# Optimization experiments

Hardware: AMD Instinct MI355X
Metric: run time of the kernel (lower is better)

## Reference

```python
import jax, jax.numpy as jnp
import numpy as np

DIM = 512
NUM_HEADS = 8
HEAD_DIM = DIM // NUM_HEADS
SCALE = HEAD_DIM ** -0.5


def setup_inputs() -> dict:
    key = jax.random.key(0)
    k_x, k_qkv, k_proj, k_pb = jax.random.split(key, 4)
    x = jax.random.normal(k_x, (2, 4096, DIM), dtype=jnp.float32)
    # nn.Linear weights: stored as [out, in]; qkv_bias=False so no qkv bias.
    w_qkv = jax.random.normal(k_qkv, (3 * DIM, DIM), dtype=jnp.float32) * (DIM ** -0.5)
    w_proj = jax.random.normal(k_proj, (DIM, DIM), dtype=jnp.float32) * (DIM ** -0.5)
    b_proj = jax.random.normal(k_pb, (DIM,), dtype=jnp.float32) * 0.01
    return {"x": x, "w_qkv": w_qkv, "w_proj": w_proj, "b_proj": b_proj}


def reference(x, w_qkv, w_proj, b_proj):
    B, N, D = x.shape
    H, Hd = NUM_HEADS, HEAD_DIM
    # qkv: [B, N, 3D] -> [3, B, H, N, Hd]
    qkv = (x @ w_qkv.T).reshape(B, N, 3, H, Hd).transpose(2, 0, 3, 1, 4)
    q, k, v = qkv[0], qkv[1], qkv[2]
    # Naive full attention matrix in fp32 (matches original non-fused path).
    attn = jnp.einsum('bhqd,bhkd->bhqk', q, k) * SCALE
    attn = jax.nn.softmax(attn, axis=-1)
    out = jnp.einsum('bhqk,bhkd->bhqd', attn, v)
    out = out.transpose(0, 2, 1, 3).reshape(B, N, D)
    return out @ w_proj.T + b_proj
```

## Files before the change

### kernel.cpp

```cpp
#include <hip/hip_runtime.h>
#include <stdint.h>

#define SEQ   4096
#define DIMM  512
#define HDIM  64
#define NH    8
#define ROWS  8192
#define QKVN  1536

typedef __attribute__((ext_vector_type(8))) __bf16 bf16x8;
typedef __attribute__((ext_vector_type(4))) float  f32x4;
typedef __attribute__((ext_vector_type(4))) uint32_t u32x4;

__device__ __forceinline__ uint32_t cvtpk(float lo, float hi) {
  uint32_t w;
  asm("v_cvt_pk_bf16_f32 %0, %1, %2" : "=v"(w) : "v"(lo), "v"(hi));
  return w;
}

__device__ __forceinline__ void swap32(uint32_t& a, uint32_t& b) {
  asm("v_permlane32_swap_b32 %0, %1" : "+v"(a), "+v"(b));
}
__device__ __forceinline__ void swap16(uint32_t& a, uint32_t& b) {
  asm("v_permlane16_swap_b32 %0, %1" : "+v"(a), "+v"(b));
}

__device__ __forceinline__ f32x4 mfma16(bf16x8 a, bf16x8 b, f32x4 c) {
  return __builtin_amdgcn_mfma_f32_16x16x32_bf16(a, b, c, 0, 0, 0);
}

#if __has_builtin(__builtin_amdgcn_exp2f)
#define EXP2F(x) __builtin_amdgcn_exp2f(x)
#else
#define EXP2F(x) exp2f(x)
#endif

__device__ __forceinline__ void gld16(const void* g, void* l) {
  __builtin_amdgcn_global_load_lds(
      (const __attribute__((address_space(1))) uint32_t*)g,
      (__attribute__((address_space(3))) uint32_t*)l, 16, 0, 0);
}

#define X4  (ROWS * DIMM / 4)
#define Q4  (QKVN * DIMM / 4)
#define P4  (DIMM * DIMM / 4)

__global__ __launch_bounds__(256) void cvt_kernel(
    const float* __restrict__ x, const float* __restrict__ wq,
    const float* __restrict__ wp, uint16_t* __restrict__ xb,
    uint16_t* __restrict__ wqb, uint16_t* __restrict__ wpb) {
  int idx = blockIdx.x * 256 + threadIdx.x;
  const float* src; uint16_t* dst; int i4;
  if (idx < X4)            { src = x;  dst = xb;  i4 = idx; }
  else if (idx < X4 + Q4)  { src = wq; dst = wqb; i4 = idx - X4; }
  else                     { src = wp; dst = wpb; i4 = idx - X4 - Q4; }
  float4 v = ((const float4*)src)[i4];
  uint2 o;
  o.x = cvtpk(v.x, v.y);
  o.y = cvtpk(v.z, v.w);
  ((uint2*)dst)[i4] = o;
}

__device__ __forceinline__ void gemm_core(
    const uint16_t* __restrict__ A, const uint16_t* __restrict__ B,
    uint16_t (*As)[128 * 32], uint16_t (*Bs)[128 * 32], f32x4 acc[4][4]) {
  const int tid = threadIdx.x;
  const int lane = tid & 63, wave = tid >> 6;
  const int quad = lane >> 4, l16 = lane & 15;
  const int wr = (wave & 1) * 64, wc = (wave >> 1) * 64;
  const int bm = blockIdx.x, bn = blockIdx.y;
  const int sw = (l16 >> 1) & 3;

  auto stage = [&](int buf, int kt) {
#pragma unroll
    for (int it = 0; it < 2; ++it) {
      int L = it * 256 + tid;
      int r = L >> 2, c = L & 3;
      int gc = c ^ ((r >> 1) & 3);
      int ldsoff = (it * 256 + (tid & ~63)) * 16;
      gld16((const char*)A + ((size_t)(bm * 128 + r) * DIMM + kt * 32) * 2 + gc * 16,
            (char*)As[buf] + ldsoff);
      gld16((const char*)B + ((size_t)(bn * 128 + r) * DIMM + kt * 32) * 2 + gc * 16,
            (char*)Bs[buf] + ldsoff);
    }
  };

  stage(0, 0);
  for (int kt = 0; kt < DIMM / 32; ++kt) {
    const int cur = kt & 1;
    __syncthreads();
    if (kt < DIMM / 32 - 1) stage(cur ^ 1, kt + 1);

    bf16x8 af[4], bfr[4];
#pragma unroll
    for (int i = 0; i < 4; ++i)
      af[i] = *(const bf16x8*)(As[cur] + (wr + i * 16 + l16) * 32 + ((quad ^ sw) * 8));
#pragma unroll
    for (int j = 0; j < 4; ++j)
      bfr[j] = *(const bf16x8*)(Bs[cur] + (wc + j * 16 + l16) * 32 + ((quad ^ sw) * 8));
    __builtin_amdgcn_s_setprio(1);
#pragma unroll
    for (int i = 0; i < 4; ++i)
#pragma unroll
      for (int j = 0; j < 4; ++j)
        acc[i][j] = mfma16(af[i], bfr[j], acc[i][j]);
    __builtin_amdgcn_s_setprio(0);
  }
}

__global__ __launch_bounds__(256, 4) void qkv_gemm(
    const uint16_t* __restrict__ xb, const uint16_t* __restrict__ wqb,
    uint16_t* __restrict__ qd, uint16_t* __restrict__ kd,
    uint16_t* __restrict__ vt) {
  __shared__ __align__(16) uint16_t As[2][128 * 32];
  __shared__ __align__(16) uint16_t Bs[2][128 * 32];
  f32x4 acc[4][4];
#pragma unroll
  for (int i = 0; i < 4; ++i)
#pragma unroll
    for (int j = 0; j < 4; ++j) acc[i][j] = f32x4{0.f, 0.f, 0.f, 0.f};

  gemm_core(xb, wqb, As, Bs, acc);

  const int lane = threadIdx.x & 63, wave = threadIdx.x >> 6;
  const int quad = lane >> 4, l16 = lane & 15;
  const int wr = (wave & 1) * 64, wc = (wave >> 1) * 64;
  const float qscale = 0.125f * 1.44269504f;
#pragma unroll
  for (int i = 0; i < 4; ++i) {
    int m0 = blockIdx.x * 128 + wr + i * 16 + quad * 4;
    int b = m0 >> 12, n0 = m0 & 4095;
#pragma unroll
    for (int j = 0; j < 4; ++j) {
      int jc = blockIdx.y * 128 + wc + j * 16 + l16;
      int region = jc >> 9;
      int h = (jc >> 6) & 7, hd = jc & 63;
      int bh = (b << 3) | h;
      if (region == 0) {
        uint32_t w01 = cvtpk(acc[i][j][0] * qscale, acc[i][j][1] * qscale);
        uint32_t w23 = cvtpk(acc[i][j][2] * qscale, acc[i][j][3] * qscale);
        size_t rb = ((size_t)bh * SEQ + n0) * HDIM + hd;
        qd[rb]            = (uint16_t)w01;
        qd[rb + HDIM]     = (uint16_t)(w01 >> 16);
        qd[rb + 2 * HDIM] = (uint16_t)w23;
        qd[rb + 3 * HDIM] = (uint16_t)(w23 >> 16);
      } else if (region == 1) {
        uint32_t w01 = cvtpk(acc[i][j][0], acc[i][j][1]);
        uint32_t w23 = cvtpk(acc[i][j][2], acc[i][j][3]);
        size_t rb = ((size_t)bh * SEQ + n0) * HDIM + hd;
        kd[rb]            = (uint16_t)w01;
        kd[rb + HDIM]     = (uint16_t)(w01 >> 16);
        kd[rb + 2 * HDIM] = (uint16_t)w23;
        kd[rb + 3 * HDIM] = (uint16_t)(w23 >> 16);
      } else {
        uint2 pk;
        pk.x = cvtpk(acc[i][j][0], acc[i][j][1]);
        pk.y = cvtpk(acc[i][j][2], acc[i][j][3]);
        *(uint2*)(vt + ((size_t)bh * HDIM + hd) * SEQ + n0) = pk;
      }
    }
  }
}

__global__ __launch_bounds__(512, 4) void attn_kernel(
    const uint16_t* __restrict__ qd, const uint16_t* __restrict__ kd,
    const uint16_t* __restrict__ vt, uint16_t* __restrict__ ao) {
  __shared__ __align__(16) uint16_t Ks[2][128 * 64];
  __shared__ __align__(16) uint16_t Vs[2][64 * 128];

  const int tid = threadIdx.x, lane = tid & 63, wave = tid >> 6;
  const int quad = lane >> 4, l16 = lane & 15;
  const int pair = wave >> 1, khalf = wave & 1;
  const int wid = blockIdx.x;
  const int xcd = wid & 7, slot = wid >> 3;
  const int bh = xcd + 8 * (slot & 1);
  const int qt = slot >> 1;
  const size_t base_qk = (size_t)bh * SEQ * HDIM;
  const size_t base_v  = (size_t)bh * HDIM * SEQ;
  const int sw7 = l16 & 7;

  auto stage = [&](int buf, int kt) {
#pragma unroll
    for (int it = 0; it < 2; ++it) {
      int L = it * 512 + tid;
      int ldsoff = (it * 512 + (tid & ~63)) * 16;
      int rk = L >> 3, ck = L & 7;
      int gck = ck ^ (rk & 7);
      gld16((const char*)kd + (base_qk + (size_t)(kt * 128 + rk) * HDIM) * 2 + gck * 16,
            (char*)Ks[buf] + ldsoff);
      int rv = L >> 4, cv = L & 15;
      int gcv = cv ^ (rv & 15);
      gld16((const char*)vt + (base_v + (size_t)rv * SEQ + (size_t)kt * 128) * 2 + gcv * 16,
            (char*)Vs[buf] + ldsoff);
    }
  };

  bf16x8 qf[2][2];
#pragma unroll
  for (int it2 = 0; it2 < 2; ++it2)
#pragma unroll
    for (int kh = 0; kh < 2; ++kh)
      qf[it2][kh] = *(const bf16x8*)(qd + base_qk +
          (size_t)(qt * 128 + pair * 32 + it2 * 16 + l16) * HDIM + kh * 32 + quad * 8);

  f32x4 O[2][4];
  float lsum[2] = {0.f, 0.f};
#pragma unroll
  for (int a = 0; a < 2; ++a)
#pragma unroll
    for (int d = 0; d < 4; ++d) O[a][d] = f32x4{0.f, 0.f, 0.f, 0.f};

  stage(0, 0);
  for (int kt = 0; kt < SEQ / 128; ++kt) {
    const int cur = kt & 1;
    __syncthreads();
    if (kt < SEQ / 128 - 1) stage(cur ^ 1, kt + 1);

    bf16x8 kf[4][2];
#pragma unroll
    for (int jh = 0; jh < 4; ++jh) {
      int jf = khalf * 4 + jh;
      const uint16_t* krow = Ks[cur] + (jf * 16 + l16) * 64;
      kf[jh][0] = *(const bf16x8*)(krow + ((quad ^ sw7) * 8));
      kf[jh][1] = *(const bf16x8*)(krow + (((4 + quad) ^ sw7) * 8));
    }

    f32x4 P[4][2];
    __builtin_amdgcn_s_setprio(1);
#pragma unroll
    for (int jh = 0; jh < 4; ++jh)
#pragma unroll
      for (int it2 = 0; it2 < 2; ++it2) {
        f32x4 s = f32x4{0.f, 0.f, 0.f, 0.f};
        s = mfma16(kf[jh][0], qf[it2][0], s);
        s = mfma16(kf[jh][1], qf[it2][1], s);
        P[jh][it2] = s;
      }
    __builtin_amdgcn_s_setprio(0);

    uint32_t sp[4][2][2];
#pragma unroll
    for (int jh = 0; jh < 4; ++jh)
#pragma unroll
      for (int it2 = 0; it2 < 2; ++it2) {
        float p0 = EXP2F(P[jh][it2][0]);
        float p1 = EXP2F(P[jh][it2][1]);
        float p2 = EXP2F(P[jh][it2][2]);
        float p3 = EXP2F(P[jh][it2][3]);
        lsum[it2] += (p0 + p1) + (p2 + p3);
        sp[jh][it2][0] = cvtpk(p0, p1);
        sp[jh][it2][1] = cvtpk(p2, p3);
      }

    bf16x8 pb[2][2];
#pragma unroll
    for (int kp = 0; kp < 2; ++kp)
#pragma unroll
      for (int it2 = 0; it2 < 2; ++it2) {
        uint32_t t0 = sp[2 * kp][it2][0], t2 = sp[2 * kp + 1][it2][0];
        swap32(t0, t2); swap16(t0, t2);
        uint32_t t1 = sp[2 * kp][it2][1], t3 = sp[2 * kp + 1][it2][1];
        swap32(t1, t3); swap16(t1, t3);
        u32x4 w = {t0, t1, t2, t3};
        pb[kp][it2] = __builtin_bit_cast(bf16x8, w);
      }

#pragma unroll
    for (int kp = 0; kp < 2; ++kp) {
      bf16x8 va[4];
#pragma unroll
      for (int dl = 0; dl < 4; ++dl)
        va[dl] = *(const bf16x8*)((const char*)Vs[cur] + (dl * 16 + l16) * 256 +
                                  (((khalf * 8 + kp * 4 + quad) ^ l16) & 15) * 16);
      __builtin_amdgcn_s_setprio(1);
#pragma unroll
      for (int it2 = 0; it2 < 2; ++it2)
#pragma unroll
        for (int dl = 0; dl < 4; ++dl)
          O[it2][dl] = mfma16(va[dl], pb[kp][it2], O[it2][dl]);
      __builtin_amdgcn_s_setprio(0);
    }
  }

  __syncthreads();
  if (!(wave & 1)) {
    f32x4* ob = (f32x4*)((char*)Ks + pair * 8192);
#pragma unroll
    for (int it2 = 0; it2 < 2; ++it2)
#pragma unroll
      for (int dl = 0; dl < 4; ++dl)
        ob[(it2 * 4 + dl) * 64 + lane] = O[it2][dl];
    float2* lb = (float2*)((char*)Vs + pair * 512);
    lb[lane] = make_float2(lsum[0], lsum[1]);
  }
  __syncthreads();
  if (wave & 1) {
    const f32x4* ob = (const f32x4*)((char*)Ks + pair * 8192);
    float2 lp = ((const float2*)((char*)Vs + pair * 512))[lane];
    lsum[0] += lp.x; lsum[1] += lp.y;
#pragma unroll
    for (int it2 = 0; it2 < 2; ++it2)
#pragma unroll
      for (int dl = 0; dl < 4; ++dl)
        O[it2][dl] += ob[(it2 * 4 + dl) * 64 + lane];

    const int b = bh >> 3, h = bh & 7;
#pragma unroll
    for (int it2 = 0; it2 < 2; ++it2) {
      float l = lsum[it2];
      l += __shfl_xor(l, 16);
      l += __shfl_xor(l, 32);
      float inv = 1.0f / l;
      int q = qt * 128 + pair * 32 + it2 * 16 + l16;
      size_t rowbase = ((size_t)(b * SEQ + q)) * DIMM + h * HDIM;
#pragma unroll
      for (int dl = 0; dl < 4; ++dl) {
        uint2 pk;
        pk.x = cvtpk(O[it2][dl][0] * inv, O[it2][dl][1] * inv);
        pk.y = cvtpk(O[it2][dl][2] * inv, O[it2][dl][3] * inv);
        *(uint2*)(ao + rowbase + dl * 16 + quad * 4) = pk;
      }
    }
  }
}

__global__ __launch_bounds__(256, 4) void proj_gemm(
    const uint16_t* __restrict__ ao, const uint16_t* __restrict__ wpb,
    const float* __restrict__ bprj, float* __restrict__ out) {
  __shared__ __align__(16) uint16_t As[2][128 * 32];
  __shared__ __align__(16) uint16_t Bs[2][128 * 32];
  f32x4 acc[4][4];
#pragma unroll
  for (int i = 0; i < 4; ++i)
#pragma unroll
    for (int j = 0; j < 4; ++j) acc[i][j] = f32x4{0.f, 0.f, 0.f, 0.f};

  gemm_core(ao, wpb, As, Bs, acc);

  const int lane = threadIdx.x & 63, wave = threadIdx.x >> 6;
  const int quad = lane >> 4, l16 = lane & 15;
  const int wr = (wave & 1) * 64, wc = (wave >> 1) * 64;
#pragma unroll
  for (int i = 0; i < 4; ++i) {
    int m0 = blockIdx.x * 128 + wr + i * 16 + quad * 4;
#pragma unroll
    for (int j = 0; j < 4; ++j) {
      int jc = blockIdx.y * 128 + wc + j * 16 + l16;
      float bias = bprj[jc];
#pragma unroll
      for (int r = 0; r < 4; ++r)
        out[(size_t)(m0 + r) * DIMM + jc] = acc[i][j][r] + bias;
    }
  }
}

extern "C" void kernel_launch(void* const* d_in, const int* in_sizes, int n_in,
                              void* d_out, int out_size, void* d_ws, size_t ws_size,
                              hipStream_t stream) {
  const float* x     = (const float*)d_in[0];
  const float* wqkv  = (const float*)d_in[1];
  const float* wproj = (const float*)d_in[2];
  const float* bproj = (const float*)d_in[3];

  char* ws = (char*)d_ws;
  uint16_t* xb  = (uint16_t*)(ws + 0);
  uint16_t* wqb = (uint16_t*)(ws + 8388608);
  uint16_t* wpb = (uint16_t*)(ws + 9961472);
  uint16_t* qd  = (uint16_t*)(ws + 10485760);
  uint16_t* kd  = (uint16_t*)(ws + 18874368);
  uint16_t* vt  = (uint16_t*)(ws + 27262976);
  uint16_t* ao  = (uint16_t*)(ws + 35651584);

  cvt_kernel<<<(X4 + Q4 + P4) / 256, 256, 0, stream>>>(x, wqkv, wproj, xb, wqb, wpb);
  qkv_gemm<<<dim3(64, 12), 256, 0, stream>>>(xb, wqb, qd, kd, vt);
  attn_kernel<<<512, 512, 0, stream>>>(qd, kd, vt, ao);
  proj_gemm<<<dim3(64, 4), 256, 0, stream>>>(ao, wpb, bproj, (float*)d_out);
}
```

Before: 183.4 us.

## Software-pipeline attention K/V loads with split staging, and remap GEMM tiles per XCD

The attention loop now stages K and V separately and keeps K two tiles ahead. The QK^T for tile t+1 is computed while the exp/pack for tile t runs, using explicit vmcnt waits and raw barriers in place of __syncthreads. This is meant to overlap global loads with MFMA and exp work and to cut barrier stalls. The QKV and projection GEMMs also remap the linear block index so tiles sharing the same row panel land on the same XCD, for better L2 reuse. The hand-counted waitcnts add a correctness risk if the in-flight load counts are wrong.

New measurement: 573.1 us. +212.5%, slower.

```diff
diff --git a/kernel.cpp b/kernel.cpp
--- a/kernel.cpp
+++ b/kernel.cpp
@@ -7,6 +7,7 @@
 #define NH    8
 #define ROWS  8192
 #define QKVN  1536
+#define NT    (SEQ / 128)
 
 typedef __attribute__((ext_vector_type(8))) __bf16 bf16x8;
 typedef __attribute__((ext_vector_type(4))) float  f32x4;
@@ -40,6 +41,12 @@
       (const __attribute__((address_space(1))) uint32_t*)g,
       (__attribute__((address_space(3))) uint32_t*)l, 16, 0, 0);
 }
+
+#define WAIT_BAR(N) do {                                      \
+    asm volatile("s_waitcnt vmcnt(" #N ")" ::: "memory");     \
+    __builtin_amdgcn_s_barrier();                             \
+    __builtin_amdgcn_sched_barrier(0);                        \
+  } while (0)
 
 #define X4  (ROWS * DIMM / 4)
 #define Q4  (QKVN * DIMM / 4)
@@ -62,13 +69,13 @@
 }
 
 __device__ __forceinline__ void gemm_core(
+    int bm, int bn,
     const uint16_t* __restrict__ A, const uint16_t* __restrict__ B,
     uint16_t (*As)[128 * 32], uint16_t (*Bs)[128 * 32], f32x4 acc[4][4]) {
   const int tid = threadIdx.x;
   const int lane = tid & 63, wave = tid >> 6;
   const int quad = lane >> 4, l16 = lane & 15;
   const int wr = (wave & 1) * 64, wc = (wave >> 1) * 64;
-  const int bm = blockIdx.x, bn = blockIdx.y;
   const int sw = (l16 >> 1) & 3;
 
   auto stage = [&](int buf, int kt) {
@@ -114,13 +121,16 @@
     uint16_t* __restrict__ vt) {
   __shared__ __align__(16) uint16_t As[2][128 * 32];
   __shared__ __align__(16) uint16_t Bs[2][128 * 32];
+  const int lin = blockIdx.y * 64 + blockIdx.x;
+  const int bm = (lin & 7) * 8 + ((lin >> 3) / 12);
+  const int bn = (lin >> 3) % 12;
   f32x4 acc[4][4];
 #pragma unroll
   for (int i = 0; i < 4; ++i)
 #pragma unroll
     for (int j = 0; j < 4; ++j) acc[i][j] = f32x4{0.f, 0.f, 0.f, 0.f};
 
-  gemm_core(xb, wqb, As, Bs, acc);
+  gemm_core(bm, bn, xb, wqb, As, Bs, acc);
 
   const int lane = threadIdx.x & 63, wave = threadIdx.x >> 6;
   const int quad = lane >> 4, l16 = lane & 15;
@@ -128,11 +138,11 @@
   const float qscale = 0.125f * 1.44269504f;
 #pragma unroll
   for (int i = 0; i < 4; ++i) {
-    int m0 = blockIdx.x * 128 + wr + i * 16 + quad * 4;
+    int m0 = bm * 128 + wr + i * 16 + quad * 4;
     int b = m0 >> 12, n0 = m0 & 4095;
 #pragma unroll
     for (int j = 0; j < 4; ++j) {
-      int jc = blockIdx.y * 128 + wc + j * 16 + l16;
+      int jc = bn * 128 + wc + j * 16 + l16;
       int region = jc >> 9;
       int h = (jc >> 6) & 7, hd = jc & 63;
       int bh = (b << 3) | h;
@@ -179,19 +189,26 @@
   const size_t base_v  = (size_t)bh * HDIM * SEQ;
   const int sw7 = l16 & 7;
 
-  auto stage = [&](int buf, int kt) {
+  auto stageK = [&](int sl, int kt) {
 #pragma unroll
     for (int it = 0; it < 2; ++it) {
       int L = it * 512 + tid;
-      int ldsoff = (it * 512 + (tid & ~63)) * 16;
       int rk = L >> 3, ck = L & 7;
       int gck = ck ^ (rk & 7);
+      int ldsoff = (it * 512 + (tid & ~63)) * 16;
       gld16((const char*)kd + (base_qk + (size_t)(kt * 128 + rk) * HDIM) * 2 + gck * 16,
-            (char*)Ks[buf] + ldsoff);
+            (char*)Ks[sl] + ldsoff);
+    }
+  };
+  auto stageV = [&](int sl, int kt) {
+#pragma unroll
+    for (int it = 0; it < 2; ++it) {
+      int L = it * 512 + tid;
       int rv = L >> 4, cv = L & 15;
       int gcv = cv ^ (rv & 15);
+      int ldsoff = (it * 512 + (tid & ~63)) * 16;
       gld16((const char*)vt + (base_v + (size_t)rv * SEQ + (size_t)kt * 128) * 2 + gcv * 16,
-            (char*)Vs[buf] + ldsoff);
+            (char*)Vs[sl] + ldsoff);
     }
   };
 
@@ -210,48 +227,39 @@
 #pragma unroll
     for (int d = 0; d < 4; ++d) O[a][d] = f32x4{0.f, 0.f, 0.f, 0.f};
 
-  stage(0, 0);
-  for (int kt = 0; kt < SEQ / 128; ++kt) {
-    const int cur = kt & 1;
-    __syncthreads();
-    if (kt < SEQ / 128 - 1) stage(cur ^ 1, kt + 1);
-
-    bf16x8 kf[4][2];
+  auto qkt = [&](int sl, f32x4 (&P)[4][2]) {
 #pragma unroll
     for (int jh = 0; jh < 4; ++jh) {
       int jf = khalf * 4 + jh;
-      const uint16_t* krow = Ks[cur] + (jf * 16 + l16) * 64;
-      kf[jh][0] = *(const bf16x8*)(krow + ((quad ^ sw7) * 8));
-      kf[jh][1] = *(const bf16x8*)(krow + (((4 + quad) ^ sw7) * 8));
-    }
-
-    f32x4 P[4][2];
-    __builtin_amdgcn_s_setprio(1);
-#pragma unroll
-    for (int jh = 0; jh < 4; ++jh)
+      const uint16_t* krow = Ks[sl] + (jf * 16 + l16) * 64;
+      bf16x8 kf0 = *(const bf16x8*)(krow + ((quad ^ sw7) * 8));
+      bf16x8 kf1 = *(const bf16x8*)(krow + (((4 + quad) ^ sw7) * 8));
 #pragma unroll
       for (int it2 = 0; it2 < 2; ++it2) {
         f32x4 s = f32x4{0.f, 0.f, 0.f, 0.f};
-        s = mfma16(kf[jh][0], qf[it2][0], s);
-        s = mfma16(kf[jh][1], qf[it2][1], s);
+        s = mfma16(kf0, qf[it2][0], s);
+        s = mfma16(kf1, qf[it2][1], s);
         P[jh][it2] = s;
       }
-    __builtin_amdgcn_s_setprio(0);
-
-    uint32_t sp[4][2][2];
+    }
+  };
+
+  auto expPack = [&](f32x4 (&Pc)[4][2], uint32_t (&sp)[4][2][2]) {
 #pragma unroll
     for (int jh = 0; jh < 4; ++jh)
 #pragma unroll
       for (int it2 = 0; it2 < 2; ++it2) {
-        float p0 = EXP2F(P[jh][it2][0]);
-        float p1 = EXP2F(P[jh][it2][1]);
-        float p2 = EXP2F(P[jh][it2][2]);
-        float p3 = EXP2F(P[jh][it2][3]);
+        float p0 = EXP2F(Pc[jh][it2][0]);
+        float p1 = EXP2F(Pc[jh][it2][1]);
+        float p2 = EXP2F(Pc[jh][it2][2]);
+        float p3 = EXP2F(Pc[jh][it2][3]);
         lsum[it2] += (p0 + p1) + (p2 + p3);
         sp[jh][it2][0] = cvtpk(p0, p1);
         sp[jh][it2][1] = cvtpk(p2, p3);
       }
-
+  };
+
+  auto pvStep = [&](int sl, uint32_t (&sp)[4][2][2]) {
     bf16x8 pb[2][2];
 #pragma unroll
     for (int kp = 0; kp < 2; ++kp)
@@ -264,13 +272,12 @@
         u32x4 w = {t0, t1, t2, t3};
         pb[kp][it2] = __builtin_bit_cast(bf16x8, w);
       }
-
 #pragma unroll
     for (int kp = 0; kp < 2; ++kp) {
       bf16x8 va[4];
 #pragma unroll
       for (int dl = 0; dl < 4; ++dl)
-        va[dl] = *(const bf16x8*)((const char*)Vs[cur] + (dl * 16 + l16) * 256 +
+        va[dl] = *(const bf16x8*)((const char*)Vs[sl] + (dl * 16 + l16) * 256 +
                                   (((khalf * 8 + kp * 4 + quad) ^ l16) & 15) * 16);
       __builtin_amdgcn_s_setprio(1);
 #pragma unroll
@@ -280,6 +287,29 @@
           O[it2][dl] = mfma16(va[dl], pb[kp][it2], O[it2][dl]);
       __builtin_amdgcn_s_setprio(0);
     }
+  };
+
+  auto stagestep = [&](int t, f32x4 (&Pc)[4][2], f32x4 (&Pn)[4][2]) {
+    WAIT_BAR(2);
+    if (t + 2 < NT) stageK(t & 1, t + 2);
+    uint32_t sp[4][2][2];
+    if (t + 1 < NT) qkt((t + 1) & 1, Pn);
+    expPack(Pc, sp);
+    if (t + 2 < NT) { WAIT_BAR(2); } else { WAIT_BAR(0); }
+    if (t + 1 < NT) stageV((t + 1) & 1, t + 1);
+    pvStep(t & 1, sp);
+  };
+
+  stageK(0, 0); stageK(1, 1); stageV(0, 0);
+  asm volatile("s_waitcnt vmcnt(4)" ::: "memory");
+  __builtin_amdgcn_s_barrier();
+  __builtin_amdgcn_sched_barrier(0);
+  f32x4 Pa[4][2], Pb[4][2];
+  qkt(0, Pa);
+
+  for (int t = 0; t < NT; t += 2) {
+    stagestep(t, Pa, Pb);
+    stagestep(t + 1, Pb, Pa);
   }
 
   __syncthreads();
@@ -329,23 +359,26 @@
     const float* __restrict__ bprj, float* __restrict__ out) {
   __shared__ __align__(16) uint16_t As[2][128 * 32];
   __shared__ __align__(16) uint16_t Bs[2][128 * 32];
+  const int lin = blockIdx.y * 64 + blockIdx.x;
+  const int bm = (lin & 7) * 8 + ((lin >> 3) >> 2);
+  const int bn = (lin >> 3) & 3;
   f32x4 acc[4][4];
 #pragma unroll
   for (int i = 0; i < 4; ++i)
 #pragma unroll
     for (int j = 0; j < 4; ++j) acc[i][j] = f32x4{0.f, 0.f, 0.f, 0.f};
 
-  gemm_core(ao, wpb, As, Bs, acc);
+  gemm_core(bm, bn, ao, wpb, As, Bs, acc);
 
   const int lane = threadIdx.x & 63, wave = threadIdx.x >> 6;
   const int quad = lane >> 4, l16 = lane & 15;
   const int wr = (wave & 1) * 64, wc = (wave >> 1) * 64;
 #pragma unroll
   for (int i = 0; i < 4; ++i) {
-    int m0 = blockIdx.x * 128 + wr + i * 16 + quad * 4;
+    int m0 = bm * 128 + wr + i * 16 + quad * 4;
 #pragma unroll
     for (int j = 0; j < 4; ++j) {
-      int jc = blockIdx.y * 128 + wc + j * 16 + l16;
+      int jc = bn * 128 + wc + j * 16 + l16;
       float bias = bprj[jc];
 #pragma unroll
       for (int r = 0; r < 4; ++r)
```

## Remap GEMM blocks for XCD locality and halve proj tile rows

Applied to the files above, without the earlier changes.

Both GEMMs now remap the linear block id so that consecutive blocks, which are spread round-robin across the 8 XCDs, share row tiles within an XCD, aiming to improve L2 reuse of A/B tiles. The projection GEMM switches to 64x128 tiles with each wave covering 32 columns, doubling the grid to 512 blocks so the 256-CU device is better filled. The smaller tile lowers per-block arithmetic intensity and adds more loads of the weight tile.

Measured after the change: 180.3 us. No clear change (-1.7%).

```diff
diff --git a/kernel.cpp b/kernel.cpp
--- a/kernel.cpp
+++ b/kernel.cpp
@@ -62,13 +62,13 @@
 }
 
 __device__ __forceinline__ void gemm_core(
+    int bm, int bn,
     const uint16_t* __restrict__ A, const uint16_t* __restrict__ B,
     uint16_t (*As)[128 * 32], uint16_t (*Bs)[128 * 32], f32x4 acc[4][4]) {
   const int tid = threadIdx.x;
   const int lane = tid & 63, wave = tid >> 6;
   const int quad = lane >> 4, l16 = lane & 15;
   const int wr = (wave & 1) * 64, wc = (wave >> 1) * 64;
-  const int bm = blockIdx.x, bn = blockIdx.y;
   const int sw = (l16 >> 1) & 3;
 
   auto stage = [&](int buf, int kt) {
@@ -114,13 +114,16 @@
     uint16_t* __restrict__ vt) {
   __shared__ __align__(16) uint16_t As[2][128 * 32];
   __shared__ __align__(16) uint16_t Bs[2][128 * 32];
+  const int lin = blockIdx.y * 64 + blockIdx.x;
+  const int bm = (lin & 7) * 8 + ((lin >> 3) / 12);
+  const int bn = (lin >> 3) % 12;
   f32x4 acc[4][4];
 #pragma unroll
   for (int i = 0; i < 4; ++i)
 #pragma unroll
     for (int j = 0; j < 4; ++j) acc[i][j] = f32x4{0.f, 0.f, 0.f, 0.f};
 
-  gemm_core(xb, wqb, As, Bs, acc);
+  gemm_core(bm, bn, xb, wqb, As, Bs, acc);
 
   const int lane = threadIdx.x & 63, wave = threadIdx.x >> 6;
   const int quad = lane >> 4, l16 = lane & 15;
@@ -128,11 +131,11 @@
   const float qscale = 0.125f * 1.44269504f;
 #pragma unroll
   for (int i = 0; i < 4; ++i) {
-    int m0 = blockIdx.x * 128 + wr + i * 16 + quad * 4;
+    int m0 = bm * 128 + wr + i * 16 + quad * 4;
     int b = m0 >> 12, n0 = m0 & 4095;
 #pragma unroll
     for (int j = 0; j < 4; ++j) {
-      int jc = blockIdx.y * 128 + wc + j * 16 + l16;
+      int jc = bn * 128 + wc + j * 16 + l16;
       int region = jc >> 9;
       int h = (jc >> 6) & 7, hd = jc & 63;
       int bh = (b << 3) | h;
@@ -327,25 +330,72 @@
 __global__ __launch_bounds__(256, 4) void proj_gemm(
     const uint16_t* __restrict__ ao, const uint16_t* __restrict__ wpb,
     const float* __restrict__ bprj, float* __restrict__ out) {
-  __shared__ __align__(16) uint16_t As[2][128 * 32];
+  __shared__ __align__(16) uint16_t As[2][64 * 32];
   __shared__ __align__(16) uint16_t Bs[2][128 * 32];
-  f32x4 acc[4][4];
+  const int lin = blockIdx.y * 128 + blockIdx.x;
+  const int idx = lin >> 3;
+  const int bm = (lin & 7) * 16 + (idx >> 2);
+  const int bn = idx & 3;
+
+  const int tid = threadIdx.x;
+  const int lane = tid & 63, wave = tid >> 6;
+  const int quad = lane >> 4, l16 = lane & 15;
+  const int wc = wave * 32;
+  const int sw = (l16 >> 1) & 3;
+
+  f32x4 acc[4][2];
 #pragma unroll
   for (int i = 0; i < 4; ++i)
 #pragma unroll
-    for (int j = 0; j < 4; ++j) acc[i][j] = f32x4{0.f, 0.f, 0.f, 0.f};
-
-  gemm_core(ao, wpb, As, Bs, acc);
-
-  const int lane = threadIdx.x & 63, wave = threadIdx.x >> 6;
-  const int quad = lane >> 4, l16 = lane & 15;
-  const int wr = (wave & 1) * 64, wc = (wave >> 1) * 64;
+    for (int j = 0; j < 2; ++j) acc[i][j] = f32x4{0.f, 0.f, 0.f, 0.f};
+
+  auto stage = [&](int buf, int kt) {
+    {
+      int r = tid >> 2, c = tid & 3;
+      int gc = c ^ ((r >> 1) & 3);
+      int ldsoff = (tid & ~63) * 16;
+      gld16((const char*)ao + ((size_t)(bm * 64 + r) * DIMM + kt * 32) * 2 + gc * 16,
+            (char*)As[buf] + ldsoff);
+    }
+#pragma unroll
+    for (int it = 0; it < 2; ++it) {
+      int L = it * 256 + tid;
+      int r = L >> 2, c = L & 3;
+      int gc = c ^ ((r >> 1) & 3);
+      int ldsoff = (it * 256 + (tid & ~63)) * 16;
+      gld16((const char*)wpb + ((size_t)(bn * 128 + r) * DIMM + kt * 32) * 2 + gc * 16,
+            (char*)Bs[buf] + ldsoff);
+    }
+  };
+
+  stage(0, 0);
+  for (int kt = 0; kt < DIMM / 32; ++kt) {
+    const int cur = kt & 1;
+    __syncthreads();
+    if (kt < DIMM / 32 - 1) stage(cur ^ 1, kt + 1);
+
+    bf16x8 af[4], bfr[2];
+#pragma unroll
+    for (int i = 0; i < 4; ++i)
+      af[i] = *(const bf16x8*)(As[cur] + (i * 16 + l16) * 32 + ((quad ^ sw) * 8));
+#pragma unroll
+    for (int j = 0; j < 2; ++j)
+      bfr[j] = *(const bf16x8*)(Bs[cur] + (wc + j * 16 + l16) * 32 + ((quad ^ sw) * 8));
+    __builtin_amdgcn_s_setprio(1);
+#pragma unroll
+    for (int i = 0; i < 4; ++i)
+#pragma unroll
+      for (int j = 0; j < 2; ++j)
+        acc[i][j] = mfma16(af[i], bfr[j], acc[i][j]);
+    __builtin_amdgcn_s_setprio(0);
+  }
+
 #pragma unroll
   for (int i = 0; i < 4; ++i) {
-    int m0 = blockIdx.x * 128 + wr + i * 16 + quad * 4;
-#pragma unroll
-    for (int j = 0; j < 4; ++j) {
-      int jc = blockIdx.y * 128 + wc + j * 16 + l16;
+    int m0 = bm * 64 + i * 16 + quad * 4;
+#pragma unroll
+    for (int j = 0; j < 2; ++j) {
+      int jc = bn * 128 + wc + j * 16 + l16;
       float bias = bprj[jc];
 #pragma unroll
       for (int r = 0; r < 4; ++r)
@@ -374,5 +424,5 @@
   cvt_kernel<<<(X4 + Q4 + P4) / 256, 256, 0, stream>>>(x, wqkv, wproj, xb, wqb, wpb);
   qkv_gemm<<<dim3(64, 12), 256, 0, stream>>>(xb, wqb, qd, kd, vt);
   attn_kernel<<<512, 512, 0, stream>>>(qd, kd, vt, ao);
-  proj_gemm<<<dim3(64, 4), 256, 0, stream>>>(ao, wpb, bproj, (float*)d_out);
-}
+  proj_gemm<<<dim3(128, 4), 256, 0, stream>>>(ao, wpb, bproj, (float*)d_out);
+}
```
